# Optimization experiments

Hardware: AMD Instinct MI355X
Metric: run time of the kernel (lower is better)

## Reference

```python
import jax, jax.numpy as jnp
import numpy as np

N = 4096
FIN = 256
FOUT = 256
H = 1  # num_heads MUST be 1: edge projections reshape [N,N,H] -> (1,N,N)
NEG_MASK = -1000000.0
LRELU_SLOPE = 0.2
ESP = 1e-06
LN_EPS = 1e-05


def setup_inputs() -> dict:
    key = jax.random.key(0)
    ks = jax.random.split(key, 9)
    nodes_features = jax.random.normal(ks[0], (N, FIN), dtype=jnp.float32)
    degree_matrix = jax.random.normal(ks[1], (N, N), dtype=jnp.float32)
    edges_features_distance = jax.random.uniform(ks[2], (N, N), dtype=jnp.float32)
    edges_features_bond = jax.random.uniform(ks[3], (N, N), dtype=jnp.float32)
    # learned parameters (xavier-ish scale)
    proj_param = jax.random.normal(ks[4], (H, FIN, FOUT), dtype=jnp.float32) * (1.0 / np.sqrt(FIN))
    a_src = jax.random.normal(ks[5], (H, FOUT, 1), dtype=jnp.float32) * (1.0 / np.sqrt(FOUT))
    a_tgt = jax.random.normal(ks[6], (H, FOUT, 1), dtype=jnp.float32) * (1.0 / np.sqrt(FOUT))
    w_dist = jax.random.normal(ks[7], (H, 1), dtype=jnp.float32)  # nn.Linear(1, H).weight
    w_bond = jax.random.normal(ks[8], (H, 1), dtype=jnp.float32)
    return {
        "nodes_features": nodes_features,
        "degree_matrix": degree_matrix,
        "edges_features_distance": edges_features_distance,
        "edges_features_bond": edges_features_bond,
        "proj_param": proj_param,
        "a_src": a_src,
        "a_tgt": a_tgt,
        "w_dist": w_dist,
        "w_bond": w_bond,
        "cutoff": 0,
    }


def reference(nodes_features, degree_matrix, edges_features_distance,
              edges_features_bond, proj_param, a_src, a_tgt, w_dist, w_bond,
              cutoff=0):
    n = nodes_features.shape[0]
    h, fin, fout = proj_param.shape
    # connectivity mask: keep degree where positive, else large negative
    connectivity_mask = jnp.where(degree_matrix > 0, degree_matrix, NEG_MASK)
    # node projection: [H, N, Fout] (dropout is identity in eval)
    proj = jnp.einsum('nf,hfo->hno', nodes_features, proj_param)
    # attention scores: outer-sum of per-node source/target scores
    s_src = jnp.einsum('hno,hoi->hni', proj, a_src)      # [H, N, 1]
    s_tgt = jnp.einsum('hno,hoi->hni', proj, a_tgt)      # [H, N, 1]
    all_scores = jax.nn.leaky_relu(s_src + jnp.swapaxes(s_tgt, 1, 2), LRELU_SLOPE)  # [H,N,N]
    # edge contributions: Linear(1, H) on scalar edge features, reshaped (1,N,N) (H==1)
    dist_c = ((-edges_features_distance)[..., None] * w_dist[:, 0]).reshape(1, n, n)
    bond_c = (edges_features_bond[..., None] * w_bond[:, 0]).reshape(1, n, n)
    all_scores = all_scores + dist_c + bond_c
    # masked softmax over neighbors
    attn = jax.nn.softmax(all_scores + connectivity_mask[None], axis=-1)  # [H,N,N]
    # weighted aggregation
    out = jnp.einsum('hnm,hmo->hno', attn, proj)  # [H, N, Fout]
    # faithful to torch: transpose(2,1) -> [H,Fout,N] then contiguous view(-1,H,Fout)
    out = jnp.transpose(out, (0, 2, 1)).reshape(-1, h, fout)
    # concat heads (skip connection and bias are disabled per init args)
    out = out.reshape(-1, h * fout)
    out = jax.nn.elu(out)  # ELU activation, alpha=1
    # ---- no_grad connectivity update ----
    o = jax.lax.stop_gradient(out)
    dm = jax.lax.stop_gradient(degree_matrix)
    sim = o @ o.T                                        # [N, N]
    decay = -jax.lax.stop_gradient(edges_features_distance)
    upd = jax.nn.sigmoid(sim) * decay * (dm > 0).astype(o.dtype)
    upd = upd + ESP
    mean = jnp.mean(upd, axis=-1, keepdims=True)
    var = jnp.mean(jnp.square(upd - mean), axis=-1, keepdims=True)
    upd = (upd - mean) / jnp.sqrt(var + LN_EPS)          # layer_norm, no affine
    upd = upd + upd.T
    return out, upd
```

## Files before the change

kernel.cpp:

```cpp
#include <hip/hip_runtime.h>


using f32x4  = __attribute__((ext_vector_type(4))) float;
using bf16x8 = __attribute__((ext_vector_type(8))) __bf16;
using bf16x4 = __attribute__((ext_vector_type(4))) __bf16;
using u32x4  = __attribute__((ext_vector_type(4))) unsigned int;

__global__ __launch_bounds__(256) void cvt_nodes_kernel(const float* __restrict__ x,
                                                        __bf16* __restrict__ y) {
  int i = (blockIdx.x * 256 + threadIdx.x) * 4;
  f32x4 v = *(const f32x4*)(x + i);
  bf16x4 o = { (__bf16)v[0], (__bf16)v[1], (__bf16)v[2], (__bf16)v[3] };
  *(bf16x4*)(y + i) = o;
}

__global__ __launch_bounds__(256) void cvt_wt_kernel(const float* __restrict__ w,
                                                     __bf16* __restrict__ wt) {
  int i = blockIdx.x * 256 + threadIdx.x;
  int o = i >> 8, f = i & 255;
  wt[i] = (__bf16)w[f * 256 + o];
}

__global__ __launch_bounds__(256) void zero_kernel(float* __restrict__ p) {
  p[blockIdx.x * 256 + threadIdx.x] = 0.0f;
}

template<int BM, int BN, int MODE>
__global__ __launch_bounds__(256) void gemm_bf16_kernel(
    const __bf16* __restrict__ A, const __bf16* __restrict__ Bt,
    int M, int N, int K,
    float* __restrict__ outf, __bf16* __restrict__ outb,
    const float* __restrict__ e0, const float* __restrict__ e1,
    const __bf16* __restrict__ axp, float* __restrict__ outt,
    float* __restrict__ bsum, float* __restrict__ bsq)
{
  constexpr int LDT = 72;
  constexpr int MI = BM / 32;
  constexpr int NI = BN / 32;
  __shared__ alignas(16) __bf16 As[BM * LDT];
  __shared__ alignas(16) __bf16 Bs[BN * LDT];
  const int tid  = threadIdx.x;
  const int lane = tid & 63;
  const int wid  = tid >> 6;
  const int wm0  = (wid >> 1) * (BM / 2);
  const int wn0  = (wid & 1) * (BN / 2);
  const int m0   = blockIdx.x * BM;
  const int n0   = blockIdx.y * BN;
  const int lr   = lane & 15;
  const int lk   = lane >> 4;

  f32x4 acc[MI][NI];
#pragma unroll
  for (int a = 0; a < MI; ++a)
#pragma unroll
    for (int b = 0; b < NI; ++b) acc[a][b] = (f32x4){0.f, 0.f, 0.f, 0.f};

  for (int kt = 0; kt < K; kt += 64) {
    __syncthreads();
    for (int idx = tid; idx < BM * 8; idx += 256) {
      int r = idx >> 3, c = idx & 7;
      u32x4 v = *(const u32x4*)(A + (size_t)(m0 + r) * K + kt + c * 8);
      *(u32x4*)(As + r * LDT + c * 8) = v;
    }
    for (int idx = tid; idx < BN * 8; idx += 256) {
      int r = idx >> 3, c = idx & 7;
      u32x4 v = *(const u32x4*)(Bt + (size_t)(n0 + r) * K + kt + c * 8);
      *(u32x4*)(Bs + r * LDT + c * 8) = v;
    }
    __syncthreads();
#pragma unroll
    for (int kk = 0; kk < 2; ++kk) {
      bf16x8 av[MI], bv[NI];
#pragma unroll
      for (int mi = 0; mi < MI; ++mi)
        av[mi] = *(const bf16x8*)(As + (wm0 + mi * 16 + lr) * LDT + kk * 32 + lk * 8);
#pragma unroll
      for (int ni = 0; ni < NI; ++ni)
        bv[ni] = *(const bf16x8*)(Bs + (wn0 + ni * 16 + lr) * LDT + kk * 32 + lk * 8);
#pragma unroll
      for (int mi = 0; mi < MI; ++mi)
#pragma unroll
        for (int ni = 0; ni < NI; ++ni)
          acc[mi][ni] = __builtin_amdgcn_mfma_f32_16x16x32_bf16(av[mi], bv[ni], acc[mi][ni], 0, 0, 0);
    }
  }

  if constexpr (MODE == 0) {
#pragma unroll
    for (int mi = 0; mi < MI; ++mi)
#pragma unroll
      for (int ni = 0; ni < NI; ++ni)
#pragma unroll
        for (int j = 0; j < 4; ++j) {
          const int m = m0 + wm0 + mi * 16 + lk * 4 + j;
          const int n = n0 + wn0 + ni * 16 + lr;
          const float v = acc[mi][ni][j];
          outf[(size_t)m * 256 + n] = v;
          outb[(size_t)n * 4096 + m] = (__bf16)v;
        }
  } else {
#pragma unroll
    for (int mi = 0; mi < MI; ++mi) {
#pragma unroll
      for (int j = 0; j < 4; ++j) {
        const int m = m0 + wm0 + mi * 16 + lk * 4 + j;
        float s = 0.f, s2 = 0.f;
#pragma unroll
        for (int ni = 0; ni < NI; ++ni) {
          const int n = n0 + wn0 + ni * 16 + lr;
          const size_t idx = (size_t)m * 4096 + n;
          const float v = acc[mi][ni][j];
          const float sg = 1.0f / (1.0f + __expf(-v));
          float tval;
          if constexpr (MODE == 2) {
            const float d = e0[idx];
            const float g = e1[idx];
            tval = sg * (-d) * (g > 0.f ? 1.0f : 0.0f) + 1e-6f;
          } else {
            const float a = (float)__builtin_nontemporal_load(axp + idx);
            tval = sg * a + 1e-6f;
          }
          outt[idx] = tval;
          s += tval;
          s2 += tval * tval;
        }
#pragma unroll
        for (int o = 1; o < 16; o <<= 1) {
          s  += __shfl_xor(s, o, 64);
          s2 += __shfl_xor(s2, o, 64);
        }
        if (lr == 0) {
          const int slot = blockIdx.y * 2 + (wid & 1);
          bsum[(size_t)slot * 4096 + m] = s;
          bsq [(size_t)slot * 4096 + m] = s2;
        }
      }
    }
  }
}

__global__ __launch_bounds__(256) void stats_small_kernel(
    const float* __restrict__ bsum, const float* __restrict__ bsq,
    float* __restrict__ mean, float* __restrict__ rstd)
{
  const int row = blockIdx.x * 256 + threadIdx.x;
  float S = 0.f, S2 = 0.f;
#pragma unroll 8
  for (int s = 0; s < 64; ++s) {
    S  += bsum[(size_t)s * 4096 + row];
    S2 += bsq [(size_t)s * 4096 + row];
  }
  const float m  = S * (1.0f / 4096.0f);
  const float var = S2 * (1.0f / 4096.0f) - m * m;
  mean[row] = m;
  rstd[row] = rsqrtf(var + 1e-5f);
}

__global__ __launch_bounds__(256) void score_exp_kernel(
    const float* __restrict__ dist, const float* __restrict__ bond,
    const float* __restrict__ deg,  const float* __restrict__ ssrc,
    const float* __restrict__ stgt, const float* __restrict__ wdp,
    const float* __restrict__ wbp,  __bf16* __restrict__ P,
    __bf16* __restrict__ aux,       float* __restrict__ Lrow)
{
  const float wd = wdp[0], wb = wbp[0];
  const int lane = threadIdx.x & 63;
  size_t i = ((size_t)blockIdx.x * 256 + threadIdx.x) * 4;
  const size_t stride = (size_t)4096 * 256 * 4;
#pragma unroll 2
  for (int it = 0; it < 4; ++it, i += stride) {
    const int row = (int)(i >> 12);
    const int col = (int)(i & 4095);
    f32x4 d  = __builtin_nontemporal_load((const f32x4*)(dist + i));
    f32x4 g  = __builtin_nontemporal_load((const f32x4*)(deg + i));
    f32x4 b  = __builtin_nontemporal_load((const f32x4*)(bond + i));
    f32x4 st = *(const f32x4*)(stgt + col);
    const float si = ssrc[row];
    f32x4 p;
    bf16x4 pb, ab;
#pragma unroll
    for (int q = 0; q < 4; ++q) {
      float x = si + st[q];
      x = x > 0.f ? x : 0.2f * x;
      x += -d[q] * wd + b[q] * wb + (g[q] > 0.f ? g[q] : -1000000.0f);
      p[q] = __expf(x);
      pb[q] = (__bf16)p[q];
      ab[q] = (__bf16)(g[q] > 0.f ? -d[q] : 0.0f);
    }
    *(bf16x4*)(P + i) = pb;
    if (aux) *(bf16x4*)(aux + i) = ab;
    float s = p[0] + p[1] + p[2] + p[3];
#pragma unroll
    for (int o = 32; o; o >>= 1) s += __shfl_xor(s, o, 64);
    if (lane == 0) atomicAdd(Lrow + row, s);
  }
}

__global__ __launch_bounds__(256) void gemm_splitk_kernel(
    const __bf16* __restrict__ A, const __bf16* __restrict__ Bt,
    __bf16* __restrict__ partial)
{
  constexpr int LDT = 72;
  __shared__ alignas(16) __bf16 As[64 * LDT];
  __shared__ alignas(16) __bf16 Bs[128 * LDT];
  const int tid  = threadIdx.x;
  const int lane = tid & 63;
  const int wid  = tid >> 6;
  const int wm0  = (wid >> 1) * 32;
  const int wn0  = (wid & 1) * 64;
  const int m0   = blockIdx.x * 64;
  const int n0   = blockIdx.y * 128;
  const int s    = blockIdx.z;
  const int lr   = lane & 15;
  const int lk   = lane >> 4;

  f32x4 acc[2][4];
#pragma unroll
  for (int a = 0; a < 2; ++a)
#pragma unroll
    for (int b = 0; b < 4; ++b) acc[a][b] = (f32x4){0.f, 0.f, 0.f, 0.f};

  const int k0 = s * 512;
  for (int kt = k0; kt < k0 + 512; kt += 64) {
    __syncthreads();
    for (int idx = tid; idx < 512; idx += 256) {
      int r = idx >> 3, c = idx & 7;
      u32x4 v = *(const u32x4*)(A + (size_t)(m0 + r) * 4096 + kt + c * 8);
      *(u32x4*)(As + r * LDT + c * 8) = v;
    }
    for (int idx = tid; idx < 1024; idx += 256) {
      int r = idx >> 3, c = idx & 7;
      u32x4 v = *(const u32x4*)(Bt + (size_t)(n0 + r) * 4096 + kt + c * 8);
      *(u32x4*)(Bs + r * LDT + c * 8) = v;
    }
    __syncthreads();
#pragma unroll
    for (int kk = 0; kk < 2; ++kk) {
      bf16x8 av[2], bv[4];
#pragma unroll
      for (int mi = 0; mi < 2; ++mi)
        av[mi] = *(const bf16x8*)(As + (wm0 + mi * 16 + lr) * LDT + kk * 32 + lk * 8);
#pragma unroll
      for (int ni = 0; ni < 4; ++ni)
        bv[ni] = *(const bf16x8*)(Bs + (wn0 + ni * 16 + lr) * LDT + kk * 32 + lk * 8);
#pragma unroll
      for (int mi = 0; mi < 2; ++mi)
#pragma unroll
        for (int ni = 0; ni < 4; ++ni)
          acc[mi][ni] = __builtin_amdgcn_mfma_f32_16x16x32_bf16(av[mi], bv[ni], acc[mi][ni], 0, 0, 0);
    }
  }

  __bf16* Pp = partial + (size_t)s * (4096 * 256);
#pragma unroll
  for (int mi = 0; mi < 2; ++mi)
#pragma unroll
    for (int ni = 0; ni < 4; ++ni)
#pragma unroll
      for (int j = 0; j < 4; ++j) {
        const int m = m0 + wm0 + mi * 16 + lk * 4 + j;
        const int n = n0 + wn0 + ni * 16 + lr;
        Pp[(size_t)m * 256 + n] = (__bf16)acc[mi][ni][j];
      }
}

__global__ __launch_bounds__(256) void reduce_elu_kernel(
    const __bf16* __restrict__ partial, const float* __restrict__ Lrow,
    float* __restrict__ out0, __bf16* __restrict__ E)
{
  __shared__ float tile[64][65];
  __shared__ float invL[64];
  const int tid = threadIdx.x;
  const int m0 = blockIdx.x * 64;
  const int f0 = blockIdx.y * 64;
  if (tid < 64) invL[tid] = 1.0f / Lrow[m0 + tid];
  f32x4 accv[4];
#pragma unroll
  for (int i = 0; i < 4; ++i) {
    int lin = i * 1024 + tid * 4;
    int r = lin >> 6, c = lin & 63;
    f32x4 sum = (f32x4){0.f, 0.f, 0.f, 0.f};
#pragma unroll
    for (int s = 0; s < 8; ++s) {
      bf16x4 pv = __builtin_nontemporal_load(
          (const bf16x4*)(partial + (size_t)s * (4096 * 256) +
                          (size_t)(m0 + r) * 256 + f0 + c));
#pragma unroll
      for (int q = 0; q < 4; ++q) sum[q] += (float)pv[q];
    }
    accv[i] = sum;
  }
  __syncthreads();
#pragma unroll
  for (int i = 0; i < 4; ++i) {
    int lin = i * 1024 + tid * 4;
    int r = lin >> 6, c = lin & 63;
    const float inv = invL[r];
    tile[r][c]     = accv[i][0] * inv;
    tile[r][c + 1] = accv[i][1] * inv;
    tile[r][c + 2] = accv[i][2] * inv;
    tile[r][c + 3] = accv[i][3] * inv;
  }
  __syncthreads();
#pragma unroll
  for (int i = 0; i < 4; ++i) {
    int lin = i * 1024 + tid * 4;
    int rr = lin >> 6, cc = lin & 63;
    f32x4 e;
#pragma unroll
    for (int q = 0; q < 4; ++q) {
      float v = tile[cc + q][rr];
      e[q] = v > 0.f ? v : expm1f(v);
    }
    size_t idx = (size_t)(f0 + rr) * 4096 + m0 + cc;
    __builtin_nontemporal_store(e, (f32x4*)(out0 + idx));
    bf16x4 eb = { (__bf16)e[0], (__bf16)e[1], (__bf16)e[2], (__bf16)e[3] };
    *(bf16x4*)(E + idx) = eb;
  }
}

__global__ __launch_bounds__(256) void sproj_kernel(const float* __restrict__ proj,
                                                    const float* __restrict__ asrc,
                                                    const float* __restrict__ atgt,
                                                    float* __restrict__ ssrc,
                                                    float* __restrict__ stgt) {
  const int row  = blockIdx.x * 4 + (threadIdx.x >> 6);
  const int lane = threadIdx.x & 63;
  f32x4 p = *(const f32x4*)(proj + (size_t)row * 256 + lane * 4);
  f32x4 a = *(const f32x4*)(asrc + lane * 4);
  f32x4 b = *(const f32x4*)(atgt + lane * 4);
  float d1 = p[0]*a[0] + p[1]*a[1] + p[2]*a[2] + p[3]*a[3];
  float d2 = p[0]*b[0] + p[1]*b[1] + p[2]*b[2] + p[3]*b[3];
#pragma unroll
  for (int o = 32; o; o >>= 1) { d1 += __shfl_xor(d1, o, 64); d2 += __shfl_xor(d2, o, 64); }
  if (lane == 0) { ssrc[row] = d1; stgt[row] = d2; }
}

__global__ __launch_bounds__(256) void finalize_kernel(float* __restrict__ t,
                                                       const float* __restrict__ mean,
                                                       const float* __restrict__ rstd) {
  const int bj = blockIdx.x, bi = blockIdx.y;
  if (bi > bj) return;
  __shared__ float ta[64][65];
  __shared__ float tb[64][65];
  const int tid = threadIdx.x;
#pragma unroll
  for (int i = 0; i < 4; ++i) {
    int lin = i * 1024 + tid * 4;
    int r = lin >> 6, c = lin & 63;
    f32x4 va = __builtin_nontemporal_load(
        (const f32x4*)(t + (size_t)(bi * 64 + r) * 4096 + bj * 64 + c));
    ta[r][c] = va[0]; ta[r][c+1] = va[1]; ta[r][c+2] = va[2]; ta[r][c+3] = va[3];
  }
  if (bi != bj) {
#pragma unroll
    for (int i = 0; i < 4; ++i) {
      int lin = i * 1024 + tid * 4;
      int r = lin >> 6, c = lin & 63;
      f32x4 vb = __builtin_nontemporal_load(
          (const f32x4*)(t + (size_t)(bj * 64 + r) * 4096 + bi * 64 + c));
      tb[r][c] = vb[0]; tb[r][c+1] = vb[1]; tb[r][c+2] = vb[2]; tb[r][c+3] = vb[3];
    }
  }
  __syncthreads();
#pragma unroll
  for (int i = 0; i < 4; ++i) {
    int lin = i * 1024 + tid * 4;
    int r = lin >> 6, c = lin & 63;
    int gi = bi * 64 + r, gj = bj * 64 + c;
    const float mi_ = mean[gi], ri_ = rstd[gi];
    f32x4 mj = *(const f32x4*)(mean + gj);
    f32x4 rj = *(const f32x4*)(rstd + gj);
    f32x4 o;
#pragma unroll
    for (int q = 0; q < 4; ++q) {
      float v = (ta[r][c + q] - mi_) * ri_;
      float w = (bi == bj) ? (ta[c + q][r] - mj[q]) * rj[q]
                           : (tb[c + q][r] - mj[q]) * rj[q];
      o[q] = v + w;
    }
    __builtin_nontemporal_store(o, (f32x4*)(t + (size_t)gi * 4096 + gj));
  }
  if (bi != bj) {
#pragma unroll
    for (int i = 0; i < 4; ++i) {
      int lin = i * 1024 + tid * 4;
      int r = lin >> 6, c = lin & 63;
      int gi = bj * 64 + r, gj = bi * 64 + c;
      const float mi_ = mean[gi], ri_ = rstd[gi];
      f32x4 mj = *(const f32x4*)(mean + gj);
      f32x4 rj = *(const f32x4*)(rstd + gj);
      f32x4 o;
#pragma unroll
      for (int q = 0; q < 4; ++q) {
        float v = (tb[r][c + q] - mi_) * ri_;
        float w = (ta[c + q][r] - mj[q]) * rj[q];
        o[q] = v + w;
      }
      __builtin_nontemporal_store(o, (f32x4*)(t + (size_t)gi * 4096 + gj));
    }
  }
}

extern "C" void kernel_launch(void* const* d_in, const int* in_sizes, int n_in,
                              void* d_out, int out_size, void* d_ws, size_t ws_size,
                              hipStream_t stream) {
  const float* nodes  = (const float*)d_in[0];
  const float* degree = (const float*)d_in[1];
  const float* dist   = (const float*)d_in[2];
  const float* bond   = (const float*)d_in[3];
  const float* W      = (const float*)d_in[4];
  const float* a_src  = (const float*)d_in[5];
  const float* a_tgt  = (const float*)d_in[6];
  const float* w_dist = (const float*)d_in[7];
  const float* w_bond = (const float*)d_in[8];

  char* ws = (char*)d_ws;
  __bf16* nodesB = (__bf16*)ws;
  __bf16* Wt     = (__bf16*)(ws + (2u << 20));
  __bf16* projT  = (__bf16*)(ws + (2u << 20) + (256u << 10));
  float*  proj   = (float*)(ws + (5u << 20));
  __bf16* E      = (__bf16*)(ws + (9u << 20));
  float*  ssrc   = (float*)(ws + (11u << 20));
  float*  stgt   = ssrc + 4096;
  float*  mean   = stgt + 4096;
  float*  rstd   = mean + 4096;
  float*  Lrow   = rstd + 4096;

  const bool useAux = ws_size >= (size_t)(48u << 20);
  __bf16* aux  = useAux ? (__bf16*)(ws + (12u << 20)) : nullptr;
  float* Bsum  = useAux ? (float*)(ws + (44u << 20))
                        : (float*)(ws + (12u << 20));
  float* Bsq   = Bsum + (size_t)64 * 4096;

  float*  out0 = (float*)d_out;
  float*  t    = out0 + (size_t)4096 * 256;
  __bf16* P    = (__bf16*)t;
  __bf16* partials = (__bf16*)((char*)t + ((size_t)32 << 20));

  cvt_nodes_kernel<<<1024, 256, 0, stream>>>(nodes, nodesB);
  cvt_wt_kernel<<<256, 256, 0, stream>>>(W, Wt);

  gemm_bf16_kernel<64, 64, 0><<<dim3(64, 4), 256, 0, stream>>>(
      nodesB, Wt, 4096, 256, 256, proj, projT,
      nullptr, nullptr, nullptr, nullptr, nullptr, nullptr);

  sproj_kernel<<<1024, 256, 0, stream>>>(proj, a_src, a_tgt, ssrc, stgt);

  zero_kernel<<<16, 256, 0, stream>>>(Lrow);

  score_exp_kernel<<<4096, 256, 0, stream>>>(dist, bond, degree, ssrc, stgt,
                                             w_dist, w_bond, P, aux, Lrow);

  gemm_splitk_kernel<<<dim3(64, 2, 8), 256, 0, stream>>>(P, projT, partials);

  reduce_elu_kernel<<<dim3(64, 4), 256, 0, stream>>>(partials, Lrow, out0, E);

  if (useAux)
    gemm_bf16_kernel<128, 128, 3><<<dim3(32, 32), 256, 0, stream>>>(
        E, E, 4096, 4096, 256, nullptr, nullptr,
        nullptr, nullptr, aux, t, Bsum, Bsq);
  else
    gemm_bf16_kernel<128, 128, 2><<<dim3(32, 32), 256, 0, stream>>>(
        E, E, 4096, 4096, 256, nullptr, nullptr,
        dist, degree, nullptr, t, Bsum, Bsq);

  stats_small_kernel<<<16, 256, 0, stream>>>(Bsum, Bsq, mean, rstd);

  finalize_kernel<<<dim3(64, 64), 256, 0, stream>>>(t, mean, rstd);
}
```

Before: 187.7 us.

## Store pre-norm update matrix in bf16 aux buffer and merge prep kernels

In the aux path, the similarity GEMM epilogue now writes the pre-layernorm update as bf16 in place over the aux buffer instead of fp32 into the output. The finalize kernel then reads bf16 and writes fp32 to the output, which roughly halves intermediate write and read traffic on the 4096x4096 matrix. Row statistics are computed from the rounded bf16 values, which adds precision loss. The two convert kernels and the zero kernel are also merged into one prep launch to cut launch overhead.

```diff
diff --git a/kernel.cpp b/kernel.cpp
--- a/kernel.cpp
+++ b/kernel.cpp
@@ -6,23 +6,24 @@
 using bf16x4 = __attribute__((ext_vector_type(4))) __bf16;
 using u32x4  = __attribute__((ext_vector_type(4))) unsigned int;
 
-__global__ __launch_bounds__(256) void cvt_nodes_kernel(const float* __restrict__ x,
-                                                        __bf16* __restrict__ y) {
-  int i = (blockIdx.x * 256 + threadIdx.x) * 4;
-  f32x4 v = *(const f32x4*)(x + i);
-  bf16x4 o = { (__bf16)v[0], (__bf16)v[1], (__bf16)v[2], (__bf16)v[3] };
-  *(bf16x4*)(y + i) = o;
-}
-
-__global__ __launch_bounds__(256) void cvt_wt_kernel(const float* __restrict__ w,
-                                                     __bf16* __restrict__ wt) {
-  int i = blockIdx.x * 256 + threadIdx.x;
-  int o = i >> 8, f = i & 255;
-  wt[i] = (__bf16)w[f * 256 + o];
-}
-
-__global__ __launch_bounds__(256) void zero_kernel(float* __restrict__ p) {
-  p[blockIdx.x * 256 + threadIdx.x] = 0.0f;
+__global__ __launch_bounds__(256) void prep_kernel(const float* __restrict__ x,
+                                                   __bf16* __restrict__ y,
+                                                   const float* __restrict__ w,
+                                                   __bf16* __restrict__ wt,
+                                                   float* __restrict__ Lrow) {
+  const int bx = blockIdx.x;
+  if (bx < 1024) {
+    int i = (bx * 256 + threadIdx.x) * 4;
+    f32x4 v = *(const f32x4*)(x + i);
+    bf16x4 o = { (__bf16)v[0], (__bf16)v[1], (__bf16)v[2], (__bf16)v[3] };
+    *(bf16x4*)(y + i) = o;
+  } else {
+    int wb = bx - 1024;
+    int i = wb * 256 + threadIdx.x;
+    int o = i >> 8, f = i & 255;
+    wt[i] = (__bf16)w[f * 256 + o];
+    if (wb < 16) Lrow[wb * 256 + threadIdx.x] = 0.0f;
+  }
 }
 
 template<int BM, int BN, int MODE>
@@ -31,7 +32,7 @@
     int M, int N, int K,
     float* __restrict__ outf, __bf16* __restrict__ outb,
     const float* __restrict__ e0, const float* __restrict__ e1,
-    const __bf16* __restrict__ axp, float* __restrict__ outt,
+    __bf16* __restrict__ axt, float* __restrict__ outt,
     float* __restrict__ bsum, float* __restrict__ bsq)
 {
   constexpr int LDT = 72;
@@ -111,18 +112,21 @@
           const size_t idx = (size_t)m * 4096 + n;
           const float v = acc[mi][ni][j];
           const float sg = 1.0f / (1.0f + __expf(-v));
-          float tval;
+          float tr;
           if constexpr (MODE == 2) {
             const float d = e0[idx];
             const float g = e1[idx];
-            tval = sg * (-d) * (g > 0.f ? 1.0f : 0.0f) + 1e-6f;
+            const float tval = sg * (-d) * (g > 0.f ? 1.0f : 0.0f) + 1e-6f;
+            outt[idx] = tval;
+            tr = tval;
           } else {
-            const float a = (float)__builtin_nontemporal_load(axp + idx);
-            tval = sg * a + 1e-6f;
+            const float a = (float)__builtin_nontemporal_load(axt + idx);
+            const __bf16 tb = (__bf16)(sg * a + 1e-6f);
+            axt[idx] = tb;
+            tr = (float)tb;
           }
-          outt[idx] = tval;
-          s += tval;
-          s2 += tval * tval;
+          s += tr;
+          s2 += tr * tr;
         }
 #pragma unroll
         for (int o = 1; o < 16; o <<= 1) {
@@ -336,30 +340,33 @@
   if (lane == 0) { ssrc[row] = d1; stgt[row] = d2; }
 }
 
-__global__ __launch_bounds__(256) void finalize_kernel(float* __restrict__ t,
-                                                       const float* __restrict__ mean,
-                                                       const float* __restrict__ rstd) {
+__global__ __launch_bounds__(256) void finalize_bf16_kernel(
+    const __bf16* __restrict__ tb, float* __restrict__ upd,
+    const float* __restrict__ mean, const float* __restrict__ rstd)
+{
   const int bj = blockIdx.x, bi = blockIdx.y;
   if (bi > bj) return;
   __shared__ float ta[64][65];
-  __shared__ float tb[64][65];
+  __shared__ float tc[64][65];
   const int tid = threadIdx.x;
 #pragma unroll
   for (int i = 0; i < 4; ++i) {
     int lin = i * 1024 + tid * 4;
     int r = lin >> 6, c = lin & 63;
-    f32x4 va = __builtin_nontemporal_load(
-        (const f32x4*)(t + (size_t)(bi * 64 + r) * 4096 + bj * 64 + c));
-    ta[r][c] = va[0]; ta[r][c+1] = va[1]; ta[r][c+2] = va[2]; ta[r][c+3] = va[3];
+    bf16x4 va = __builtin_nontemporal_load(
+        (const bf16x4*)(tb + (size_t)(bi * 64 + r) * 4096 + bj * 64 + c));
+    ta[r][c] = (float)va[0]; ta[r][c+1] = (float)va[1];
+    ta[r][c+2] = (float)va[2]; ta[r][c+3] = (float)va[3];
   }
   if (bi != bj) {
 #pragma unroll
     for (int i = 0; i < 4; ++i) {
       int lin = i * 1024 + tid * 4;
       int r = lin >> 6, c = lin & 63;
-      f32x4 vb = __builtin_nontemporal_load(
-          (const f32x4*)(t + (size_t)(bj * 64 + r) * 4096 + bi * 64 + c));
-      tb[r][c] = vb[0]; tb[r][c+1] = vb[1]; tb[r][c+2] = vb[2]; tb[r][c+3] = vb[3];
+      bf16x4 vb = __builtin_nontemporal_load(
+          (const bf16x4*)(tb + (size_t)(bj * 64 + r) * 4096 + bi * 64 + c));
+      tc[r][c] = (float)vb[0]; tc[r][c+1] = (float)vb[1];
+      tc[r][c+2] = (float)vb[2]; tc[r][c+3] = (float)vb[3];
     }
   }
   __syncthreads();
@@ -376,10 +383,10 @@
     for (int q = 0; q < 4; ++q) {
       float v = (ta[r][c + q] - mi_) * ri_;
       float w = (bi == bj) ? (ta[c + q][r] - mj[q]) * rj[q]
-                           : (tb[c + q][r] - mj[q]) * rj[q];
+                           : (tc[c + q][r] - mj[q]) * rj[q];
       o[q] = v + w;
     }
-    __builtin_nontemporal_store(o, (f32x4*)(t + (size_t)gi * 4096 + gj));
+    __builtin_nontemporal_store(o, (f32x4*)(upd + (size_t)gi * 4096 + gj));
   }
   if (bi != bj) {
 #pragma unroll
@@ -393,11 +400,76 @@
       f32x4 o;
 #pragma unroll
       for (int q = 0; q < 4; ++q) {
-        float v = (tb[r][c + q] - mi_) * ri_;
+        float v = (tc[r][c + q] - mi_) * ri_;
         float w = (ta[c + q][r] - mj[q]) * rj[q];
         o[q] = v + w;
       }
-      __builtin_nontemporal_store(o, (f32x4*)(t + (size_t)gi * 4096 + gj));
+      __builtin_nontemporal_store(o, (f32x4*)(upd + (size_t)gi * 4096 + gj));
+    }
+  }
+}
+
+__global__ __launch_bounds__(256) void finalize_f32_kernel(
+    float* __restrict__ t, const float* __restrict__ mean,
+    const float* __restrict__ rstd)
+{
+  const int bj = blockIdx.x, bi = blockIdx.y;
+  if (bi > bj) return;
+  __shared__ float ta[64][65];
+  __shared__ float tc[64][65];
+  const int tid = threadIdx.x;
+#pragma unroll
+  for (int i = 0; i < 4; ++i) {
+    int lin = i * 1024 + tid * 4;
+    int r = lin >> 6, c = lin & 63;
+    f32x4 va = *(const f32x4*)(t + (size_t)(bi * 64 + r) * 4096 + bj * 64 + c);
+    ta[r][c] = va[0]; ta[r][c+1] = va[1]; ta[r][c+2] = va[2]; ta[r][c+3] = va[3];
+  }
+  if (bi != bj) {
+#pragma unroll
+    for (int i = 0; i < 4; ++i) {
+      int lin = i * 1024 + tid * 4;
+      int r = lin >> 6, c = lin & 63;
+      f32x4 vb = *(const f32x4*)(t + (size_t)(bj * 64 + r) * 4096 + bi * 64 + c);
+      tc[r][c] = vb[0]; tc[r][c+1] = vb[1]; tc[r][c+2] = vb[2]; tc[r][c+3] = vb[3];
+    }
+  }
+  __syncthreads();
+#pragma unroll
+  for (int i = 0; i < 4; ++i) {
+    int lin = i * 1024 + tid * 4;
+    int r = lin >> 6, c = lin & 63;
+    int gi = bi * 64 + r, gj = bj * 64 + c;
+    const float mi_ = mean[gi], ri_ = rstd[gi];
+    f32x4 mj = *(const f32x4*)(mean + gj);
+    f32x4 rj = *(const f32x4*)(rstd + gj);
+    f32x4 o;
+#pragma unroll
+    for (int q = 0; q < 4; ++q) {
+      float v = (ta[r][c + q] - mi_) * ri_;
+      float w = (bi == bj) ? (ta[c + q][r] - mj[q]) * rj[q]
+                           : (tc[c + q][r] - mj[q]) * rj[q];
+      o[q] = v + w;
+    }
+    *(f32x4*)(t + (size_t)gi * 4096 + gj) = o;
+  }
+  if (bi != bj) {
+#pragma unroll
+    for (int i = 0; i < 4; ++i) {
+      int lin = i * 1024 + tid * 4;
+      int r = lin >> 6, c = lin & 63;
+      int gi = bj * 64 + r, gj = bi * 64 + c;
+      const float mi_ = mean[gi], ri_ = rstd[gi];
+      f32x4 mj = *(const f32x4*)(mean + gj);
+      f32x4 rj = *(const f32x4*)(rstd + gj);
+      f32x4 o;
+#pragma unroll
+      for (int q = 0; q < 4; ++q) {
+        float v = (tc[r][c + q] - mi_) * ri_;
+        float w = (ta[c + q][r] - mj[q]) * rj[q];
+        o[q] = v + w;
+      }
+      *(f32x4*)(t + (size_t)gi * 4096 + gj) = o;
     }
   }
 }
@@ -438,8 +510,7 @@
   __bf16* P    = (__bf16*)t;
   __bf16* partials = (__bf16*)((char*)t + ((size_t)32 << 20));
 
-  cvt_nodes_kernel<<<1024, 256, 0, stream>>>(nodes, nodesB);
-  cvt_wt_kernel<<<256, 256, 0, stream>>>(W, Wt);
+  prep_kernel<<<1280, 256, 0, stream>>>(nodes, nodesB, W, Wt, Lrow);
 
   gemm_bf16_kernel<64, 64, 0><<<dim3(64, 4), 256, 0, stream>>>(
       nodesB, Wt, 4096, 256, 256, proj, projT,
@@ -447,8 +518,6 @@
 
   sproj_kernel<<<1024, 256, 0, stream>>>(proj, a_src, a_tgt, ssrc, stgt);
 
-  zero_kernel<<<16, 256, 0, stream>>>(Lrow);
-
   score_exp_kernel<<<4096, 256, 0, stream>>>(dist, bond, degree, ssrc, stgt,
                                              w_dist, w_bond, P, aux, Lrow);
 
@@ -456,16 +525,17 @@
 
   reduce_elu_kernel<<<dim3(64, 4), 256, 0, stream>>>(partials, Lrow, out0, E);
 
-  if (useAux)
+  if (useAux) {
     gemm_bf16_kernel<128, 128, 3><<<dim3(32, 32), 256, 0, stream>>>(
         E, E, 4096, 4096, 256, nullptr, nullptr,
-        nullptr, nullptr, aux, t, Bsum, Bsq);
-  else
+        nullptr, nullptr, aux, nullptr, Bsum, Bsq);
+    stats_small_kernel<<<16, 256, 0, stream>>>(Bsum, Bsq, mean, rstd);
+    finalize_bf16_kernel<<<dim3(64, 64), 256, 0, stream>>>(aux, t, mean, rstd);
+  } else {
     gemm_bf16_kernel<128, 128, 2><<<dim3(32, 32), 256, 0, stream>>>(
         E, E, 4096, 4096, 256, nullptr, nullptr,
         dist, degree, nullptr, t, Bsum, Bsq);
-
-  stats_small_kernel<<<16, 256, 0, stream>>>(Bsum, Bsq, mean, rstd);
-
-  finalize_kernel<<<dim3(64, 64), 256, 0, stream>>>(t, mean, rstd);
-}
+    stats_small_kernel<<<16, 256, 0, stream>>>(Bsum, Bsq, mean, rstd);
+    finalize_f32_kernel<<<dim3(64, 64), 256, 0, stream>>>(t, mean, rstd);
+  }
+}
```

After: 181.1 us. 3.5% less time.
